# Performance work log

Hardware: AMD Instinct MI355X
Metric: run time of the kernel (lower is better)

Reference implementation:

```python
import jax, jax.numpy as jnp
import numpy as np

EPS = 1e-5  # torch BatchNorm2d default eps


def _conv(x, w, b, pad):
    y = jax.lax.conv_general_dilated(
        x, w, window_strides=(1, 1), padding=[(pad, pad), (pad, pad)],
        dimension_numbers=('NCHW', 'OIHW', 'NCHW'))
    return y + b[None, :, None, None]


def _bn_train(x, gamma, beta):
    # training-mode BatchNorm2d: biased batch statistics over (N,H,W)
    m = jnp.mean(x, axis=(0, 2, 3), keepdims=True)
    v = jnp.var(x, axis=(0, 2, 3), keepdims=True)
    xn = (x - m) * jax.lax.rsqrt(v + EPS)
    return xn * gamma[None, :, None, None] + beta[None, :, None, None]


def _ncc(s, t):
    # Vectorized equivalent of the per-pixel double loop.
    # ncc[b,0,i,j] = mean(tt * ss / (tt_std * ss_std)) over (C,th,tw)
    #             = sum(tt * s_sub) / (N * tt_std * ss_std)   (since sum(tt)=0)
    b, c, sh, sw = s.shape
    th, tw = t.shape[2], t.shape[3]
    N = c * th * tw
    tt = t - jnp.mean(t, axis=(1, 2, 3), keepdims=True)
    # torch.std is unbiased (divides by N-1)
    tt_std = jnp.sqrt(jnp.sum(tt * tt, axis=(1, 2, 3), keepdims=True) / (N - 1))

    # cross[b] = valid correlation of s[b] with its own template tt[b]
    def per_sample(si, ti):
        return jax.lax.conv_general_dilated(
            si[None], ti[None], (1, 1), 'VALID',
            dimension_numbers=('NCHW', 'OIHW', 'NCHW'))[0]  # (1,h,w)

    cross = jax.vmap(per_sample)(s, tt)  # (b,1,h,w)

    # per-window mean/std of s via box-filter conv over all C channels jointly
    box = jnp.ones((1, c, th, tw), dtype=s.dtype)
    win_sum = jax.lax.conv_general_dilated(
        s, box, (1, 1), 'VALID', dimension_numbers=('NCHW', 'OIHW', 'NCHW'))
    win_sqsum = jax.lax.conv_general_dilated(
        s * s, box, (1, 1), 'VALID', dimension_numbers=('NCHW', 'OIHW', 'NCHW'))
    win_mean = win_sum / N
    ss_var = jnp.maximum(win_sqsum - N * win_mean * win_mean, 0.0) / (N - 1)
    ss_std = jnp.sqrt(ss_var)

    return cross / (N * tt_std * ss_std)  # (b,1,h,w)


def reference(s, t, w1, b1, g1, be1, w2, b2, g2, be2,
              w3, b3, g3, be3, w4, b4):
    s = _bn_train(_conv(s, w1, b1, pad=1), g1, be1)
    t = _bn_train(_conv(t, w2, b2, pad=1), g2, be2)
    ncc = _ncc(s, t)
    x = _bn_train(_conv(ncc, w3, b3, pad=0), g3, be3)
    x = jax.nn.relu(x)
    return _conv(x, w4, b4, pad=0)  # (b,2,h,w)


def setup_inputs() -> dict:
    key = jax.random.key(0)
    ks = jax.random.split(key, 12)
    C = 256
    inp = {
        's': jax.random.normal(ks[0], (16, C, 64, 64), jnp.float32),
        't': jax.random.normal(ks[1], (16, C, 16, 16), jnp.float32),
        'w1': jax.random.normal(ks[2], (C, C, 3, 3), jnp.float32) * 0.02,
        'b1': jax.random.normal(ks[3], (C,), jnp.float32) * 0.02,
        'g1': jnp.ones((C,), jnp.float32),
        'be1': jnp.zeros((C,), jnp.float32),
        'w2': jax.random.normal(ks[4], (C, C, 3, 3), jnp.float32) * 0.02,
        'b2': jax.random.normal(ks[5], (C,), jnp.float32) * 0.02,
        'g2': jnp.ones((C,), jnp.float32),
        'be2': jnp.zeros((C,), jnp.float32),
        'w3': jax.random.normal(ks[6], (1, 1, 1, 1), jnp.float32),
        'b3': jax.random.normal(ks[7], (1,), jnp.float32) * 0.02,
        'g3': jnp.ones((1,), jnp.float32),
        'be3': jnp.zeros((1,), jnp.float32),
        'w4': jax.random.normal(ks[8], (2, 1, 1, 1), jnp.float32),
        'b4': jax.random.normal(ks[9], (2,), jnp.float32) * 0.02,
    }
    return inp
```

## Files before the change

### kernel.cpp

```cpp
#include <hip/hip_runtime.h>
#include <hip/hip_bf16.h>

#define EPSV 1e-5f

constexpr int B_ = 16, C_ = 256;
constexpr int OHW_ = 49 * 49;
constexpr int NTOT = 256 * 16 * 16;
constexpr int GROUPS = 32, CPERG = 8;

typedef short bf16x8 __attribute__((ext_vector_type(8)));
typedef float f32x4 __attribute__((ext_vector_type(4)));

constexpr size_t OFF_S1 = 0;
constexpr size_t SZ_S1  = (size_t)16 * 256 * 4096;
constexpr size_t OFF_T2 = OFF_S1 + SZ_S1;
constexpr size_t SZ_T2  = (size_t)16 * 256 * 256;
constexpr size_t OFF_ST = OFF_T2 + SZ_T2;
constexpr size_t OFF_C  = OFF_ST + 2048;
constexpr size_t SPC_BYTES = (size_t)16 * 66 * 66 * 256 * 2;
constexpr size_t TPC_BYTES = (size_t)16 * 18 * 18 * 256 * 2;
constexpr size_t WR_BYTES  = (size_t)9 * 256 * 256 * 2;
constexpr size_t ZOFF  = 0;
constexpr size_t CPOFF = 131072;
constexpr size_t NCOFF = CPOFF + (size_t)GROUPS * 16 * OHW_;
constexpr size_t SATOFF = NCOFF + (size_t)16 * OHW_;

__device__ __forceinline__ void gload_lds16(const void* g, void* l) {
    __builtin_amdgcn_global_load_lds((const __attribute__((address_space(1))) unsigned int*)g,
                                     (__attribute__((address_space(3))) unsigned int*)l,
                                     16, 0, 0);
}

template<int W>
__global__ __launch_bounds__(256)
void pad_transpose(const float* __restrict__ in, __hip_bfloat16* __restrict__ outp)
{
    constexpr int PW = W + 2;
    __shared__ float tile[64][W + 1];
    int bid = blockIdx.x;
    int icg = bid & 3; bid >>= 2;
    int yp = bid % PW; bid /= PW;
    int b = bid;
    int ic0 = icg * 64;
    int tid = threadIdx.x;
    bool interior = (yp >= 1 && yp <= W);
    if (interior) {
        int y = yp - 1;
        for (int idx = tid; idx < 64 * W; idx += 256) {
            int i = idx / W, x = idx % W;
            tile[i][x] = in[(((size_t)(b * C_ + ic0 + i)) * W + y) * W + x];
        }
    }
    __syncthreads();
    for (int idx = tid; idx < PW * 16; idx += 256) {
        int xp = idx >> 4, i4 = idx & 15;
        ushort4 v = make_ushort4(0, 0, 0, 0);
        if (interior && xp >= 1 && xp <= W) {
            #pragma unroll
            for (int k = 0; k < 4; ++k) {
                __hip_bfloat16 h = __float2bfloat16(tile[i4 * 4 + k][xp - 1]);
                reinterpret_cast<unsigned short*>(&v)[k] = *reinterpret_cast<unsigned short*>(&h);
            }
        }
        *reinterpret_cast<ushort4*>(&outp[(((size_t)(b * PW) + yp) * PW + xp) * 256 + ic0 + i4 * 4]) = v;
    }
}

__global__ __launch_bounds__(256)
void weight_reorg(const float* __restrict__ w, __hip_bfloat16* __restrict__ wr)
{
    int idx = blockIdx.x * 256 + threadIdx.x;
    const float* src = w + (size_t)idx * 9;
    #pragma unroll
    for (int t = 0; t < 9; ++t)
        wr[(size_t)t * 65536 + idx] = __float2bfloat16(src[t]);
}

template<int W>
__global__ __launch_bounds__(256, 4)
void conv_mfma(const __hip_bfloat16* __restrict__ SPc, const __hip_bfloat16* __restrict__ Wr,
               const float* __restrict__ bias, float* __restrict__ out,
               float* __restrict__ csum, float* __restrict__ csq)
{
    constexpr int PW = W + 2;
    constexpr int NPIX = W * W;
    constexpr int NT = NPIX / 128;
    constexpr int NWG = 16 * 2 * NT;
    constexpr int CHUNK = NWG / 8;
    __shared__ __hip_bfloat16 A_lds[2][128 * 32];
    __shared__ __hip_bfloat16 B_lds[2][128 * 32];

    int logical = (blockIdx.x & 7) * CHUNK + (blockIdx.x >> 3);
    int nt = logical % NT; logical /= NT;
    int mt = logical & 1;  logical >>= 1;
    int b  = logical;
    int tid = threadIdx.x;
    int lane = tid & 63;
    int wv = tid >> 6, wm = wv >> 1, wn = wv & 1;
    int oc0 = mt * 128, p0 = nt * 128;

    f32x4 acc[4][4];
    #pragma unroll
    for (int i = 0; i < 4; ++i)
        #pragma unroll
        for (int j = 0; j < 4; ++j)
            #pragma unroll
            for (int r = 0; r < 4; ++r) acc[i][j][r] = 0.f;

    int colb = lane >> 4;
    int rA = lane & 15;
    int s_row[2], s_seg[2];
    #pragma unroll
    for (int it = 0; it < 2; ++it) {
        int sIdx = tid + it * 256;
        s_row[it] = sIdx >> 2;
        s_seg[it] = (sIdx & 3) ^ (s_row[it] & 3);
    }

    auto STAGE = [&](int buf, int kc) {
        int tap = kc >> 3, icc = kc & 7;
        int ic0 = icc * 32;
        int dy = tap / 3, dx = tap - dy * 3;
        #pragma unroll
        for (int it = 0; it < 2; ++it) {
            int sIdx = tid + it * 256;
            int row = s_row[it], sw = s_seg[it];
            const __hip_bfloat16* srcA =
                Wr + ((size_t)(tap * 256 + oc0 + row)) * 256 + ic0 + sw * 8;
            gload_lds16(srcA, &A_lds[buf][sIdx * 8]);
            int p = p0 + row;
            int y = p / W, x = p % W;
            const __hip_bfloat16* srcB =
                SPc + (((size_t)(b * PW + y + dy)) * PW + x + dx) * 256 + ic0 + sw * 8;
            gload_lds16(srcB, &B_lds[buf][sIdx * 8]);
        }
    };

    STAGE(0, 0);
    asm volatile("s_waitcnt vmcnt(0)" ::: "memory");
    __syncthreads();

    for (int kc = 0; kc < 72; ++kc) {
        int cur = kc & 1;
        if (kc + 1 < 72) STAGE(cur ^ 1, kc + 1);

        const bf16x8* Af = reinterpret_cast<const bf16x8*>(A_lds[cur]);
        const bf16x8* Bf = reinterpret_cast<const bf16x8*>(B_lds[cur]);
        bf16x8 a[4], bb[4];
        #pragma unroll
        for (int mi = 0; mi < 4; ++mi) {
            int rowA = wm * 64 + mi * 16 + rA;
            a[mi] = Af[rowA * 4 + (colb ^ (rowA & 3))];
        }
        #pragma unroll
        for (int ni = 0; ni < 4; ++ni) {
            int rowB = wn * 64 + ni * 16 + rA;
            bb[ni] = Bf[rowB * 4 + (colb ^ (rowB & 3))];
        }
        #pragma unroll
        for (int mi = 0; mi < 4; ++mi)
            #pragma unroll
            for (int ni = 0; ni < 4; ++ni)
                acc[mi][ni] = __builtin_amdgcn_mfma_f32_16x16x32_bf16(
                    a[mi], bb[ni], acc[mi][ni], 0, 0, 0);

        asm volatile("s_waitcnt vmcnt(0)" ::: "memory");
        __syncthreads();
    }

    #pragma unroll
    for (int mi = 0; mi < 4; ++mi) {
        int ocb = oc0 + wm * 64 + mi * 16 + (lane >> 4) * 4;
        #pragma unroll
        for (int r = 0; r < 4; ++r) {
            int oc = ocb + r;
            float bv = bias[oc];
            float* orow = out + ((size_t)(b * C_ + oc)) * NPIX;
            float s_oc = 0.f, q_oc = 0.f;
            #pragma unroll
            for (int ni = 0; ni < 4; ++ni) {
                int px = p0 + wn * 64 + ni * 16 + (lane & 15);
                float v = acc[mi][ni][r] + bv;
                orow[px] = v;
                s_oc += v; q_oc += v * v;
            }
            #pragma unroll
            for (int m_ = 1; m_ < 16; m_ <<= 1) {
                s_oc += __shfl_xor(s_oc, m_);
                q_oc += __shfl_xor(q_oc, m_);
            }
            if ((lane & 15) == 0) {
                atomicAdd(&csum[oc], s_oc);
                atomicAdd(&csq[oc], q_oc);
            }
        }
    }
}

__device__ inline void blk_reduce2(float& a, float& q, int tid) {
    #pragma unroll
    for (int off = 32; off > 0; off >>= 1) {
        a += __shfl_down(a, off);
        q += __shfl_down(q, off);
    }
    __shared__ float ra[4], rq[4];
    if ((tid & 63) == 0) { ra[tid >> 6] = a; rq[tid >> 6] = q; }
    __syncthreads();
    if (tid == 0) { a = ra[0] + ra[1] + ra[2] + ra[3]; q = rq[0] + rq[1] + rq[2] + rq[3]; }
}

__global__ __launch_bounds__(256)
void bn_norm(float* __restrict__ x, const float* __restrict__ csum,
             const float* __restrict__ csq, const float* __restrict__ g,
             const float* __restrict__ be, int HW, int total4, float inv_cnt)
{
    int i = blockIdx.x * 256 + threadIdx.x;
    if (i >= total4) return;
    int c = ((i * 4) / HW) % C_;
    float m = csum[c] * inv_cnt;
    float v = csq[c] * inv_cnt - m * m;
    float sc = rsqrtf(v + EPSV) * g[c];
    float sh = be[c] - m * sc;
    float4 val = reinterpret_cast<float4*>(x)[i];
    val.x = val.x * sc + sh;
    val.y = val.y * sc + sh;
    val.z = val.z * sc + sh;
    val.w = val.w * sc + sh;
    reinterpret_cast<float4*>(x)[i] = val;
}

__global__ __launch_bounds__(256)
void zplane_kernel(const float* __restrict__ s1, const float* __restrict__ csum,
                   const float* __restrict__ csq, const float* __restrict__ g1,
                   const float* __restrict__ be1, float* __restrict__ z)
{
    __shared__ float SC[256], SH[256];
    int tid = threadIdx.x;
    {
        float m = csum[tid] * (1.f / 65536.f);
        float v = csq[tid] * (1.f / 65536.f) - m * m;
        float sc = rsqrtf(v + EPSV) * g1[tid];
        SC[tid] = sc; SH[tid] = be1[tid] - m * sc;
    }
    __syncthreads();
    int i4 = blockIdx.x * 256 + tid;
    int b = i4 >> 10, p4 = i4 & 1023;
    const float4* base = reinterpret_cast<const float4*>(s1 + (size_t)b * (C_ * 4096)) + p4;
    float4 s = make_float4(0.f, 0.f, 0.f, 0.f);
    float4 q = make_float4(0.f, 0.f, 0.f, 0.f);
    for (int c = 0; c < C_; ++c) {
        float4 v = base[(size_t)c * 1024];
        float sc = SC[c], sh = SH[c];
        float vx = v.x * sc + sh, vy = v.y * sc + sh, vz = v.z * sc + sh, vw = v.w * sc + sh;
        s.x += vx; s.y += vy; s.z += vz; s.w += vw;
        q.x += vx * vx; q.y += vy * vy; q.z += vz * vz; q.w += vw * vw;
    }
    reinterpret_cast<float4*>(z)[i4] = s;
    reinterpret_cast<float4*>(z + 65536)[i4] = q;
}

__global__ __launch_bounds__(256)
void sat_kernel(const float* __restrict__ zin, float* __restrict__ sat)
{
    __shared__ float t[65][66];
    int pl = blockIdx.x;
    int tid = threadIdx.x;
    const float* src = zin + (size_t)pl * 4096;
    for (int idx = tid; idx < 4096; idx += 256) {
        int y = idx >> 6, x = idx & 63;
        t[y + 1][x + 1] = src[idx];
    }
    for (int idx = tid; idx < 65; idx += 256) { t[0][idx] = 0.f; t[idx][0] = 0.f; }
    __syncthreads();
    if (tid < 64) {
        float run = 0.f;
        for (int x = 1; x <= 64; ++x) { run += t[tid + 1][x]; t[tid + 1][x] = run; }
    }
    __syncthreads();
    if (tid < 64) {
        float run = 0.f;
        for (int y = 1; y <= 64; ++y) { run += t[y][tid + 1]; t[y][tid + 1] = run; }
    }
    __syncthreads();
    float* dst = sat + (size_t)pl * 4225;
    for (int idx = tid; idx < 4225; idx += 256) {
        int r = idx / 65, c = idx % 65;
        dst[idx] = t[r][c];
    }
}

__global__ __launch_bounds__(256)
void tstat_kernel(const float* __restrict__ t2, float* __restrict__ tmean, float* __restrict__ ttstd)
{
    int b = blockIdx.x, tid = threadIdx.x;
    const float* p = t2 + (size_t)b * NTOT;
    float s = 0.f, q = 0.f;
    for (int i = tid; i < NTOT; i += 256) { float v = p[i]; s += v; q += v * v; }
    blk_reduce2(s, q, tid);
    if (tid == 0) {
        float m = s / (float)NTOT;
        tmean[b] = m;
        ttstd[b] = sqrtf(fmaxf(q - (float)NTOT * m * m, 0.f) / (float)(NTOT - 1));
    }
}

__global__ __launch_bounds__(256, 2)
void cross_v3(const float* __restrict__ s1, const float* __restrict__ t2,
              const float* __restrict__ csum, const float* __restrict__ csq,
              const float* __restrict__ g1, const float* __restrict__ be1,
              float* __restrict__ cpart)
{
    __shared__ float4 spl4[1024];
    __shared__ float tpl[256];
    __shared__ float red[4][64][49];

    int g = blockIdx.x & (GROUPS - 1);
    int b = blockIdx.x / GROUPS;
    int tid = threadIdx.x;
    int phase = tid >> 6;
    int lane = tid & 63;
    int i = lane;
    int i_ld = i < 49 ? i : 48;

    float acc[49];
    #pragma unroll
    for (int j = 0; j < 49; ++j) acc[j] = 0.f;

    #pragma unroll 1
    for (int cc = 0; cc < CPERG; ++cc) {
        int c = g * CPERG + cc;
        float m = csum[c] * (1.f / 65536.f);
        float v = csq[c] * (1.f / 65536.f) - m * m;
        float sc = rsqrtf(v + EPSV) * g1[c];
        float sh = be1[c] - m * sc;
        __syncthreads();
        const float4* sp4 = reinterpret_cast<const float4*>(s1 + ((size_t)(b * C_ + c)) * 4096);
        #pragma unroll
        for (int k = 0; k < 4; ++k) {
            int gidx = tid + k * 256;
            float4 val = sp4[gidx];
            val.x = val.x * sc + sh; val.y = val.y * sc + sh;
            val.z = val.z * sc + sh; val.w = val.w * sc + sh;
            int row = gidx >> 4, jg = gidx & 15;
            spl4[row * 16 + (jg ^ (row & 7))] = val;
        }
        tpl[tid] = t2[((size_t)(b * C_ + c)) * 256 + tid];
        __syncthreads();
        #pragma unroll 1
        for (int tyl = 0; tyl < 4; ++tyl) {
            int ty = phase * 4 + tyl;
            int row = i_ld + ty;
            float r_[64];
            #pragma unroll
            for (int jg = 0; jg < 16; ++jg) {
                float4 v4 = spl4[row * 16 + (jg ^ (row & 7))];
                r_[jg * 4 + 0] = v4.x; r_[jg * 4 + 1] = v4.y;
                r_[jg * 4 + 2] = v4.z; r_[jg * 4 + 3] = v4.w;
            }
            float tt[16];
            const float4* tp4 = reinterpret_cast<const float4*>(&tpl[ty * 16]);
            #pragma unroll
            for (int k = 0; k < 4; ++k) {
                float4 tv = tp4[k];
                tt[k * 4 + 0] = tv.x; tt[k * 4 + 1] = tv.y;
                tt[k * 4 + 2] = tv.z; tt[k * 4 + 3] = tv.w;
            }
            #pragma unroll
            for (int tx = 0; tx < 16; ++tx)
                #pragma unroll
                for (int j = 0; j < 49; ++j)
                    acc[j] += tt[tx] * r_[j + tx];
        }
    }
    __syncthreads();
    if (i < 49) {
        #pragma unroll
        for (int j = 0; j < 49; ++j) red[phase][i][j] = acc[j];
    }
    __syncthreads();
    float* dst = cpart + ((size_t)(g * B_ + b)) * OHW_;
    for (int e = tid; e < OHW_; e += 256) {
        int ii = e / 49, jj = e - ii * 49;
        dst[e] = red[0][ii][jj] + red[1][ii][jj] + red[2][ii][jj] + red[3][ii][jj];
    }
}

__global__ __launch_bounds__(256)
void ncc_kernel(const float* __restrict__ cpart, const float* __restrict__ sat,
                const float* __restrict__ tmean, const float* __restrict__ ttstd,
                float* __restrict__ ncc, float* __restrict__ s3)
{
    int idx = blockIdx.x * 256 + threadIdx.x;
    float val = 0.f;
    if (idx < B_ * OHW_) {
        int b = idx / OHW_, r = idx - b * OHW_;
        int i = r / 49, j = r - i * 49;
        float cr = 0.f;
        #pragma unroll 4
        for (int g = 0; g < GROUPS; ++g) cr += cpart[((size_t)(g * B_ + b)) * OHW_ + r];
        const float* sz = sat + (size_t)b * 4225;
        const float* sq = sat + (size_t)(16 + b) * 4225;
        int a00 = i * 65 + j, a01 = i * 65 + j + 16;
        int a10 = (i + 16) * 65 + j, a11 = (i + 16) * 65 + j + 16;
        float wsum = sz[a11] - sz[a01] - sz[a10] + sz[a00];
        float wq   = sq[a11] - sq[a01] - sq[a10] + sq[a00];
        float crosst = cr - tmean[b] * wsum;
        float ssvar = fmaxf(wq - wsum * wsum * (1.f / 65536.f), 0.f) * (1.f / 65535.f);
        float ssstd = sqrtf(ssvar);
        val = crosst / (65536.f * ttstd[b] * ssstd);
        ncc[idx] = val;
    }
    float s = val, q = val * val;
    blk_reduce2(s, q, threadIdx.x);
    if (threadIdx.x == 0) { atomicAdd(&s3[0], s); atomicAdd(&s3[1], q); }
}

__global__ __launch_bounds__(256)
void final_kernel(const float* __restrict__ ncc, const float* __restrict__ s3,
                  const float* __restrict__ w3, const float* __restrict__ b3,
                  const float* __restrict__ g3, const float* __restrict__ be3,
                  const float* __restrict__ w4, const float* __restrict__ b4,
                  float* __restrict__ out)
{
    int idx = blockIdx.x * 256 + threadIdx.x;
    if (idx >= B_ * OHW_) return;
    constexpr float M = (float)(B_ * OHW_);
    float mn = s3[0] / M;
    float vn = s3[1] / M - mn * mn;
    float W3 = w3[0], B3 = b3[0];
    float my = W3 * mn + B3;
    float vy = W3 * W3 * vn;
    float sc = rsqrtf(vy + EPSV) * g3[0];
    float y = (W3 * ncc[idx] + B3 - my) * sc + be3[0];
    float h = fmaxf(y, 0.f);
    int b = idx / OHW_, r = idx - b * OHW_;
    out[((size_t)(b * 2 + 0)) * OHW_ + r] = h * w4[0] + b4[0];
    out[((size_t)(b * 2 + 1)) * OHW_ + r] = h * w4[1] + b4[1];
}

extern "C" void kernel_launch(void* const* d_in, const int* in_sizes, int n_in,
                              void* d_out, int out_size, void* d_ws, size_t ws_size,
                              hipStream_t stream)
{
    const float* s   = (const float*)d_in[0];
    const float* t   = (const float*)d_in[1];
    const float* w1  = (const float*)d_in[2];
    const float* b1  = (const float*)d_in[3];
    const float* g1  = (const float*)d_in[4];
    const float* be1 = (const float*)d_in[5];
    const float* w2  = (const float*)d_in[6];
    const float* b2  = (const float*)d_in[7];
    const float* g2  = (const float*)d_in[8];
    const float* be2 = (const float*)d_in[9];
    const float* w3  = (const float*)d_in[10];
    const float* b3  = (const float*)d_in[11];
    const float* g3  = (const float*)d_in[12];
    const float* be3 = (const float*)d_in[13];
    const float* w4  = (const float*)d_in[14];
    const float* b4  = (const float*)d_in[15];

    float* ws = (float*)d_ws;
    float* S1 = ws + OFF_S1;
    float* T2 = ws + OFF_T2;
    float* ST = ws + OFF_ST;
    float* CHS1 = ST + 0;
    float* CHQ1 = ST + 256;
    float* CHS2 = ST + 512;
    float* CHQ2 = ST + 768;
    float* S3   = ST + 1024;
    float* TM   = ST + 1040;
    float* TSD  = ST + 1056;

    char* Cb = (char*)(ws + OFF_C);
    __hip_bfloat16* SPc = (__hip_bfloat16*)Cb;
    __hip_bfloat16* TPc = (__hip_bfloat16*)(Cb + SPC_BYTES);
    __hip_bfloat16* Wr1 = (__hip_bfloat16*)(Cb + SPC_BYTES + TPC_BYTES);
    __hip_bfloat16* Wr2 = (__hip_bfloat16*)(Cb + SPC_BYTES + TPC_BYTES + WR_BYTES);
    float* Cf = (float*)Cb;
    float* Z   = Cf + ZOFF;
    float* CP  = Cf + CPOFF;
    float* NC  = Cf + NCOFF;
    float* SAT = Cf + SATOFF;

    hipMemsetAsync(ST, 0, 1026 * sizeof(float), stream);

    pad_transpose<64><<<dim3(16 * 66 * 4), dim3(256), 0, stream>>>(s, SPc);
    pad_transpose<16><<<dim3(16 * 18 * 4), dim3(256), 0, stream>>>(t, TPc);
    weight_reorg<<<dim3(256), dim3(256), 0, stream>>>(w1, Wr1);
    weight_reorg<<<dim3(256), dim3(256), 0, stream>>>(w2, Wr2);

    conv_mfma<64><<<dim3(16 * 2 * 32), dim3(256), 0, stream>>>(SPc, Wr1, b1, S1, CHS1, CHQ1);
    conv_mfma<16><<<dim3(16 * 2 * 2),  dim3(256), 0, stream>>>(TPc, Wr2, b2, T2, CHS2, CHQ2);

    bn_norm<<<dim3(1024), dim3(256), 0, stream>>>(T2, CHS2, CHQ2, g2, be2, 256, 262144, 1.f / 4096.f);
    tstat_kernel<<<dim3(16), dim3(256), 0, stream>>>(T2, TM, TSD);

    zplane_kernel<<<dim3(64), dim3(256), 0, stream>>>(S1, CHS1, CHQ1, g1, be1, Z);
    sat_kernel<<<dim3(32), dim3(256), 0, stream>>>(Z, SAT);

    cross_v3<<<dim3(16 * GROUPS), dim3(256), 0, stream>>>(S1, T2, CHS1, CHQ1, g1, be1, CP);
    ncc_kernel<<<dim3(151), dim3(256), 0, stream>>>(CP, SAT, TM, TSD, NC, S3);
    final_kernel<<<dim3(151), dim3(256), 0, stream>>>(NC, S3, w3, b3, g3, be3, w4, b4, (float*)d_out);
}
```

Before: 492.2 us.

## Triple-buffer conv MFMA LDS staging with one barrier per K step

The implicit-GEMM conv kernel moves from double to triple LDS buffering. Loads are issued two K-steps ahead, and the loop waits on a partial vmcnt with a single barrier per iteration instead of waiting for everything twice. Global addresses are precomputed per thread so each stage only adds a per-tap offset, and the XOR swizzle on LDS reads is removed. The larger LDS footprint lowers occupancy to 3 workgroups per CU, and dropping the swizzle may bring back LDS bank conflicts. The stage for k+2 is issued after the single barrier into the buffer consumed at k-1, so it could overwrite data a slower wave is still reading.

```diff
diff --git a/kernel.cpp b/kernel.cpp
--- a/kernel.cpp
+++ b/kernel.cpp
@@ -77,7 +77,7 @@
 }
 
 template<int W>
-__global__ __launch_bounds__(256, 4)
+__global__ __launch_bounds__(256, 3)
 void conv_mfma(const __hip_bfloat16* __restrict__ SPc, const __hip_bfloat16* __restrict__ Wr,
                const float* __restrict__ bias, float* __restrict__ out,
                float* __restrict__ csum, float* __restrict__ csq)
@@ -87,8 +87,9 @@
     constexpr int NT = NPIX / 128;
     constexpr int NWG = 16 * 2 * NT;
     constexpr int CHUNK = NWG / 8;
-    __shared__ __hip_bfloat16 A_lds[2][128 * 32];
-    __shared__ __hip_bfloat16 B_lds[2][128 * 32];
+    constexpr int NK = 72;
+    __shared__ __hip_bfloat16 A_lds[3][128 * 32];
+    __shared__ __hip_bfloat16 B_lds[3][128 * 32];
 
     int logical = (blockIdx.x & 7) * CHUNK + (blockIdx.x >> 3);
     int nt = logical % NT; logical /= NT;
@@ -109,54 +110,50 @@
 
     int colb = lane >> 4;
     int rA = lane & 15;
-    int s_row[2], s_seg[2];
+
+    const __hip_bfloat16* baseA[2];
+    const __hip_bfloat16* baseB[2];
     #pragma unroll
     for (int it = 0; it < 2; ++it) {
         int sIdx = tid + it * 256;
-        s_row[it] = sIdx >> 2;
-        s_seg[it] = (sIdx & 3) ^ (s_row[it] & 3);
+        int row = sIdx >> 2, seg = sIdx & 3;
+        baseA[it] = Wr + ((size_t)(oc0 + row)) * 256 + seg * 8;
+        int p = p0 + row;
+        int y = p / W, x = p % W;
+        baseB[it] = SPc + (((size_t)(b * PW + y)) * PW + x) * 256 + seg * 8;
     }
 
     auto STAGE = [&](int buf, int kc) {
         int tap = kc >> 3, icc = kc & 7;
-        int ic0 = icc * 32;
-        int dy = tap / 3, dx = tap - dy * 3;
+        int offA = tap * 65536 + icc * 32;
+        int offB = ((tap / 3) * PW + (tap % 3)) * 256 + icc * 32;
         #pragma unroll
         for (int it = 0; it < 2; ++it) {
             int sIdx = tid + it * 256;
-            int row = s_row[it], sw = s_seg[it];
-            const __hip_bfloat16* srcA =
-                Wr + ((size_t)(tap * 256 + oc0 + row)) * 256 + ic0 + sw * 8;
-            gload_lds16(srcA, &A_lds[buf][sIdx * 8]);
-            int p = p0 + row;
-            int y = p / W, x = p % W;
-            const __hip_bfloat16* srcB =
-                SPc + (((size_t)(b * PW + y + dy)) * PW + x + dx) * 256 + ic0 + sw * 8;
-            gload_lds16(srcB, &B_lds[buf][sIdx * 8]);
+            gload_lds16(baseA[it] + offA, &A_lds[buf][sIdx * 8]);
+            gload_lds16(baseB[it] + offB, &B_lds[buf][sIdx * 8]);
         }
     };
 
     STAGE(0, 0);
-    asm volatile("s_waitcnt vmcnt(0)" ::: "memory");
-    __syncthreads();
-
-    for (int kc = 0; kc < 72; ++kc) {
-        int cur = kc & 1;
-        if (kc + 1 < 72) STAGE(cur ^ 1, kc + 1);
-
-        const bf16x8* Af = reinterpret_cast<const bf16x8*>(A_lds[cur]);
-        const bf16x8* Bf = reinterpret_cast<const bf16x8*>(B_lds[cur]);
+    STAGE(1, 1);
+
+    for (int k = 0; k < NK; ++k) {
+        int cur = k % 3;
+        if (k + 2 < NK) { asm volatile("s_waitcnt vmcnt(4)" ::: "memory"); }
+        else            { asm volatile("s_waitcnt vmcnt(0)" ::: "memory"); }
+        __builtin_amdgcn_s_barrier();
+        asm volatile("" ::: "memory");
+
+        const bf16x8* Af = reinterpret_cast<const bf16x8*>(&A_lds[cur][0]);
+        const bf16x8* Bf = reinterpret_cast<const bf16x8*>(&B_lds[cur][0]);
         bf16x8 a[4], bb[4];
         #pragma unroll
-        for (int mi = 0; mi < 4; ++mi) {
-            int rowA = wm * 64 + mi * 16 + rA;
-            a[mi] = Af[rowA * 4 + (colb ^ (rowA & 3))];
-        }
-        #pragma unroll
-        for (int ni = 0; ni < 4; ++ni) {
-            int rowB = wn * 64 + ni * 16 + rA;
-            bb[ni] = Bf[rowB * 4 + (colb ^ (rowB & 3))];
-        }
+        for (int mi = 0; mi < 4; ++mi)
+            a[mi] = Af[(wm * 64 + mi * 16 + rA) * 4 + colb];
+        #pragma unroll
+        for (int ni = 0; ni < 4; ++ni)
+            bb[ni] = Bf[(wn * 64 + ni * 16 + rA) * 4 + colb];
         #pragma unroll
         for (int mi = 0; mi < 4; ++mi)
             #pragma unroll
@@ -164,8 +161,7 @@
                 acc[mi][ni] = __builtin_amdgcn_mfma_f32_16x16x32_bf16(
                     a[mi], bb[ni], acc[mi][ni], 0, 0, 0);
 
-        asm volatile("s_waitcnt vmcnt(0)" ::: "memory");
-        __syncthreads();
+        if (k + 2 < NK) STAGE((k + 2) % 3, k + 2);
     }
 
     #pragma unroll
```

Result: slower. 513.3 us (+4.3%).
